# Kernel optimization log

Hardware: AMD Instinct MI355X
Metric: run time of the kernel (lower is better)

The kernel has to match this reference:

```python
import jax, jax.numpy as jnp
import numpy as np

N_NODES = 50000
N_EDGES = 800000
IN_F = 128
HID = 64
HEADS = 4
OUT_F = 16
NEG_SLOPE = 0.2
BN_EPS = 1e-5


def setup_inputs() -> dict:
    key = jax.random.key(0)
    ks = jax.random.split(key, 16)
    g = lambda k, s: (jax.random.normal(k, s, dtype=jnp.float32) * 0.05)
    inp = {
        'x': jax.random.normal(ks[0], (N_NODES, IN_F), dtype=jnp.float32),
        'edge_index': jax.random.randint(ks[1], (2, N_EDGES), 0, N_NODES, dtype=jnp.int64),
        # layer 1: GATConv(128 -> 64, heads=4, concat)
        'W1': g(ks[2], (IN_F, HEADS * HID)),
        'as1': g(ks[3], (HEADS, HID)), 'ad1': g(ks[4], (HEADS, HID)),
        'b1': jnp.zeros((HEADS * HID,), jnp.float32),
        'g1': jnp.ones((HEADS * HID,), jnp.float32), 'be1': jnp.zeros((HEADS * HID,), jnp.float32),
        'm1': jnp.zeros((HEADS * HID,), jnp.float32), 'v1': jnp.ones((HEADS * HID,), jnp.float32),
        # layer 2: GATConv(256 -> 64, heads=4, concat)
        'W2': g(ks[5], (HEADS * HID, HEADS * HID)),
        'as2': g(ks[6], (HEADS, HID)), 'ad2': g(ks[7], (HEADS, HID)),
        'b2': jnp.zeros((HEADS * HID,), jnp.float32),
        'g2': jnp.ones((HEADS * HID,), jnp.float32), 'be2': jnp.zeros((HEADS * HID,), jnp.float32),
        'm2': jnp.zeros((HEADS * HID,), jnp.float32), 'v2': jnp.ones((HEADS * HID,), jnp.float32),
        # layer 3: GATConv(256 -> 16, heads=1, concat=False)
        'W3': g(ks[8], (HEADS * HID, OUT_F)),
        'as3': g(ks[9], (1, OUT_F)), 'ad3': g(ks[10], (1, OUT_F)),
        'b3': jnp.zeros((OUT_F,), jnp.float32),
    }
    return inp


def gat_conv(x, src, dst, W, a_src, a_dst, b, concat):
    n = x.shape[0]
    H, C = a_src.shape
    h = (x @ W).reshape(n, H, C)                       # [N,H,C]
    s_node = jnp.sum(h * a_src[None], axis=-1)         # [N,H]
    d_node = jnp.sum(h * a_dst[None], axis=-1)         # [N,H]
    e = jax.nn.leaky_relu(s_node[src] + d_node[dst], NEG_SLOPE)   # [E,H]
    # segment softmax over incoming edges of each dst node
    e_max = jax.ops.segment_max(e, dst, num_segments=n)
    e_exp = jnp.exp(e - e_max[dst])
    denom = jax.ops.segment_sum(e_exp, dst, num_segments=n)
    alpha = e_exp / denom[dst]                         # [E,H]
    msg = h[src] * alpha[:, :, None]                   # [E,H,C]
    out = jax.ops.segment_sum(msg, dst, num_segments=n)  # [N,H,C]
    out = out.reshape(n, H * C) if concat else out.mean(axis=1)
    return out + b


def batchnorm(x, gamma, beta, mean, var):
    return (x - mean) * jax.lax.rsqrt(var + BN_EPS) * gamma + beta


def reference(x, edge_index, W1, as1, ad1, b1, g1, be1, m1, v1,
              W2, as2, ad2, b2, g2, be2, m2, v2, W3, as3, ad3, b3):
    n = x.shape[0]
    loops = jnp.arange(n, dtype=edge_index.dtype)
    src = jnp.concatenate([edge_index[0], loops])      # PyG add_self_loops
    dst = jnp.concatenate([edge_index[1], loops])
    h = gat_conv(x, src, dst, W1, as1, ad1, b1, concat=True)
    h = jax.nn.relu(batchnorm(h, g1, be1, m1, v1))
    h = gat_conv(h, src, dst, W2, as2, ad2, b2, concat=True)
    h = jax.nn.relu(batchnorm(h, g2, be2, m2, v2))
    out = gat_conv(h, src, dst, W3, as3, ad3, b3, concat=False)
    return out  # out_channels=16 != 1 -> no sigmoid
```

## Files before the change

kernel.cpp:

```cpp
#include <hip/hip_runtime.h>
#include <math.h>

#define NN 50000
#define NE 800000
#define ET (NE + NN)
#define F1 256
#define NEG 0.2f
#define BN_EPS 1e-5f

typedef __attribute__((ext_vector_type(8))) short short8;
typedef __attribute__((ext_vector_type(4))) float float4v;
typedef __attribute__((ext_vector_type(2))) float float2v;
typedef __attribute__((ext_vector_type(4))) unsigned short ushort4v;

__device__ __forceinline__ float bf2f(unsigned short u) {
    unsigned int x = ((unsigned int)u) << 16;
    return __builtin_bit_cast(float, x);
}
__device__ __forceinline__ unsigned short f2bf(float f) {
    unsigned int x = __builtin_bit_cast(unsigned int, f);
    unsigned int lsb = (x >> 16) & 1u;
    x += 0x7fffu + lsb;
    return (unsigned short)(x >> 16);
}
__device__ __forceinline__ unsigned char f2fp8(float f) {
    int p = __builtin_amdgcn_cvt_pk_fp8_f32(f, f, 0, false);
    return (unsigned char)(p & 0xff);
}
__device__ __forceinline__ float lrelu(float x) { return x > 0.f ? x : NEG * x; }

__device__ __forceinline__ void gl_lds16(const unsigned short* g, unsigned short* l) {
    __builtin_amdgcn_global_load_lds((const __attribute__((address_space(1))) void*)g,
                                     (__attribute__((address_space(3))) void*)l, 16, 0, 0);
}

__global__ void prep_all(const float* __restrict__ x, unsigned short* __restrict__ xb,
                         const int* __restrict__ ei, int* __restrict__ counts, int* __restrict__ rank,
                         const float* __restrict__ W1, unsigned short* __restrict__ W1t,
                         const float* __restrict__ W2, unsigned short* __restrict__ W2t,
                         const float* __restrict__ W3, unsigned short* __restrict__ W3h,
                         unsigned short* __restrict__ W3l,
                         const float* __restrict__ b1, const float* __restrict__ g1,
                         const float* __restrict__ be1, const float* __restrict__ m1,
                         const float* __restrict__ v1, float* __restrict__ S1, float* __restrict__ T1,
                         const float* __restrict__ b2, const float* __restrict__ g2,
                         const float* __restrict__ be2, const float* __restrict__ m2,
                         const float* __restrict__ v2, float* __restrict__ S2, float* __restrict__ T2) {
    int blk = blockIdx.x, tid = threadIdx.x;
    if (blk < 6250) {
        int i = blk * 256 + tid;
        float4 v = ((const float4*)x)[i];
        ushort4 o;
        o.x = f2bf(v.x); o.y = f2bf(v.y); o.z = f2bf(v.z); o.w = f2bf(v.w);
        ((ushort4*)xb)[i] = o;
    } else if (blk < 9571) {
        int e = (blk - 6250) * 256 + tid;
        if (e < ET) {
            int dst = (e < NE) ? ei[NE + e] : (e - NE);
            rank[e] = atomicAdd(&counts[dst], 1);
        }
    } else if (blk < 9699) {
        int id = (blk - 9571) * 256 + tid;
        int n = id >> 7, k = id & 127;
        W1t[id] = f2bf(W1[k * 256 + n]);
    } else if (blk < 9955) {
        int id = (blk - 9699) * 256 + tid;
        int n = id >> 8, k = id & 255;
        W2t[id] = f2bf(W2[k * 256 + n]);
    } else if (blk < 9971) {
        int id = (blk - 9955) * 256 + tid;
        int n = id >> 8, k = id & 255;
        float v = W3[k * 16 + n];
        unsigned short hi = f2bf(v);
        W3h[id] = hi;
        W3l[id] = f2bf(v - bf2f(hi));
    } else if (blk == 9971) {
        float s = g1[tid] * rsqrtf(v1[tid] + BN_EPS);
        S1[tid] = s;
        T1[tid] = (b1[tid] - m1[tid]) * s + be1[tid];
    } else {
        float s = g2[tid] * rsqrtf(v2[tid] + BN_EPS);
        S2[tid] = s;
        T2[tid] = (b2[tid] - m2[tid]) * s + be2[tid];
    }
}

__global__ void scan_a(const int* __restrict__ counts, int* __restrict__ rowptr, int* __restrict__ bsum) {
    __shared__ int s[256];
    int t = threadIdx.x, i = blockIdx.x * 256 + t;
    int v = (i < NN) ? counts[i] : 0;
    s[t] = v;
    __syncthreads();
    for (int off = 1; off < 256; off <<= 1) {
        int add = (t >= off) ? s[t - off] : 0;
        __syncthreads();
        s[t] += add;
        __syncthreads();
    }
    if (i < NN) rowptr[i + 1] = s[t];
    if (t == 255) bsum[blockIdx.x] = s[255];
}

__global__ void scan_b(int* __restrict__ bsum, int nb) {
    __shared__ int s[256];
    int t = threadIdx.x;
    int v = (t < nb) ? bsum[t] : 0;
    s[t] = v;
    __syncthreads();
    for (int off = 1; off < 256; off <<= 1) {
        int add = (t >= off) ? s[t - off] : 0;
        __syncthreads();
        s[t] += add;
        __syncthreads();
    }
    if (t < nb) bsum[t] = s[t] - v;
}

__global__ void scan_c(int* __restrict__ rowptr, const int* __restrict__ bsum) {
    int i = blockIdx.x * 256 + threadIdx.x;
    if (i < NN) rowptr[i + 1] += bsum[i >> 8];
    if (i == 0) rowptr[0] = 0;
}

__global__ void edge_place(const int* __restrict__ ei, const int* __restrict__ rowptr,
                           const int* __restrict__ rank, int* __restrict__ csr) {
    int e = blockIdx.x * 256 + threadIdx.x;
    if (e < ET) {
        int src, dst;
        if (e < NE) { src = ei[e]; dst = ei[NE + e]; }
        else        { src = e - NE; dst = src; }
        csr[rowptr[dst] + rank[e]] = src;
    }
}

template<int K, bool F8OUT>
__global__ __launch_bounds__(256, 3) void gemm_lds(const unsigned short* __restrict__ A,
                                                   const unsigned short* __restrict__ Bt,
                                                   void* __restrict__ Cout,
                                                   const float* __restrict__ a_s,
                                                   const float* __restrict__ a_d,
                                                   float* __restrict__ s_arr,
                                                   float* __restrict__ d_arr,
                                                   int M) {
    __shared__ __align__(16) unsigned short As[128 * 64];
    __shared__ __align__(16) unsigned short Bs[128 * 64];
    int tid = threadIdx.x, lane = tid & 63, w = tid >> 6;
    int wr = w >> 1, wc = w & 1;
    int mBase = blockIdx.x * 128, nBase = blockIdx.y * 128;
    int lm = lane & 15, q = lane >> 4;

    float4v acc[4][4];
    for (int i = 0; i < 4; ++i)
        for (int j = 0; j < 4; ++j)
            acc[i][j] = (float4v){0.f, 0.f, 0.f, 0.f};

    const unsigned short* Ap[4];
    const unsigned short* Bp[4];
    for (int p = 0; p < 4; ++p) {
        int slot = p * 256 + tid;
        int row = slot >> 3;
        int csrc = (slot & 7) ^ (row & 7);
        int gm = mBase + row; if (gm >= M) gm = M - 1;
        Ap[p] = A + (size_t)gm * K + csrc * 8;
        Bp[p] = Bt + (size_t)(nBase + row) * K + csrc * 8;
    }

    for (int k0 = 0; k0 < K; k0 += 64) {
        #pragma unroll
        for (int p = 0; p < 4; ++p)
            gl_lds16(Ap[p] + k0, As + ((size_t)p * 256 + w * 64) * 8);
        #pragma unroll
        for (int p = 0; p < 4; ++p)
            gl_lds16(Bp[p] + k0, Bs + ((size_t)p * 256 + w * 64) * 8);
        __syncthreads();
        #pragma unroll
        for (int ks = 0; ks < 64; ks += 32) {
            int cb = ks >> 3;
            short8 af[4], bfr[4];
            #pragma unroll
            for (int i = 0; i < 4; ++i) {
                int row = wr * 64 + i * 16 + lm;
                int ch = (cb + q) ^ (row & 7);
                af[i] = *(const short8*)(As + row * 64 + ch * 8);
            }
            #pragma unroll
            for (int j = 0; j < 4; ++j) {
                int row = wc * 64 + j * 16 + lm;
                int ch = (cb + q) ^ (row & 7);
                bfr[j] = *(const short8*)(Bs + row * 64 + ch * 8);
            }
            #pragma unroll
            for (int i = 0; i < 4; ++i)
                #pragma unroll
                for (int j = 0; j < 4; ++j)
                    acc[i][j] = __builtin_amdgcn_mfma_f32_16x16x32_bf16(af[i], bfr[j], acc[i][j], 0, 0, 0);
        }
        __syncthreads();
    }

    for (int i = 0; i < 4; ++i)
        for (int j = 0; j < 4; ++j) {
            int col = nBase + wc * 64 + j * 16 + lm;
            for (int r = 0; r < 4; ++r) {
                int row = mBase + wr * 64 + i * 16 + q * 4 + r;
                if (row < M) {
                    if constexpr (F8OUT)
                        ((unsigned char*)Cout)[(size_t)row * 256 + col] = f2fp8(acc[i][j][r]);
                    else
                        ((unsigned short*)Cout)[(size_t)row * 256 + col] = f2bf(acc[i][j][r]);
                }
            }
        }
    int head = blockIdx.y * 2 + wc;
    float as_j[4], ad_j[4];
    for (int j = 0; j < 4; ++j) {
        as_j[j] = a_s[head * 64 + j * 16 + lm];
        ad_j[j] = a_d[head * 64 + j * 16 + lm];
    }
    for (int i = 0; i < 4; ++i)
        for (int r = 0; r < 4; ++r) {
            float sp = acc[i][0][r] * as_j[0] + acc[i][1][r] * as_j[1]
                     + acc[i][2][r] * as_j[2] + acc[i][3][r] * as_j[3];
            float dp = acc[i][0][r] * ad_j[0] + acc[i][1][r] * ad_j[1]
                     + acc[i][2][r] * ad_j[2] + acc[i][3][r] * ad_j[3];
            for (int off = 1; off < 16; off <<= 1) {
                sp += __shfl_xor(sp, off);
                dp += __shfl_xor(dp, off);
            }
            int row = mBase + wr * 64 + i * 16 + q * 4 + r;
            if (lm == 0 && row < M) {
                s_arr[row * 4 + head] = sp;
                d_arr[row * 4 + head] = dp;
            }
        }
}

__global__ __launch_bounds__(256) void agg12_f8(const unsigned char* __restrict__ h8,
                                                const float* __restrict__ s_arr, const float* __restrict__ d_arr,
                                                const int* __restrict__ rowptr, const int* __restrict__ csr,
                                                const float* __restrict__ S, const float* __restrict__ T,
                                                unsigned short* __restrict__ out) {
    __shared__ float wls[4][64 * 5];
    int lane = threadIdx.x & 63;
    int wv = threadIdx.x >> 6;
    int node = blockIdx.x * 4 + wv;
    if (node >= NN) return;
    int r0 = rowptr[node], r1 = rowptr[node + 1];
    float4 dv = *(const float4*)(d_arr + node * 4);
    float* wbuf = &wls[wv][0];
    int lp = lane & 31;
    int half = lane >> 5;
    int head8 = lp >> 3;
    const unsigned char* hbase = h8 + lp * 8;

    float2v a01 = {0.f, 0.f}, a23 = {0.f, 0.f}, a45 = {0.f, 0.f}, a67 = {0.f, 0.f};
    float den0 = 0.f, den1 = 0.f, den2 = 0.f, den3 = 0.f;

    for (int base = r0; base < r1; base += 64) {
        int cnt = min(64, r1 - base);
        if (lane < cnt) {
            int src = csr[base + lane];
            float4 sv = *(const float4*)(s_arr + src * 4);
            float w0 = __expf(lrelu(sv.x + dv.x));
            float w1 = __expf(lrelu(sv.y + dv.y));
            float w2 = __expf(lrelu(sv.z + dv.z));
            float w3 = __expf(lrelu(sv.w + dv.w));
            den0 += w0; den1 += w1; den2 += w2; den3 += w3;
            float* wp = wbuf + lane * 5;
            wp[0] = w0; wp[1] = w1; wp[2] = w2; wp[3] = w3;
            wp[4] = __int_as_float(src);
        } else if (lane == cnt) {
            float* wp = wbuf + lane * 5;
            wp[0] = 0.f; wp[1] = 0.f; wp[2] = 0.f; wp[3] = 0.f;
            wp[4] = __int_as_float(node);
        }
        int cpad = (cnt + 1) & ~1;
        for (int k = 0; k < cpad; k += 2) {
            const float* wp = wbuf + (k + half) * 5;
            int src = __float_as_int(wp[4]);
            float wgt = wp[head8];
            uint2 hv = *(const uint2*)(hbase + (size_t)src * 256);
            float2v c0 = __builtin_amdgcn_cvt_pk_f32_fp8((int)hv.x, false);
            float2v c1 = __builtin_amdgcn_cvt_pk_f32_fp8((int)hv.x, true);
            float2v c2 = __builtin_amdgcn_cvt_pk_f32_fp8((int)hv.y, false);
            float2v c3 = __builtin_amdgcn_cvt_pk_f32_fp8((int)hv.y, true);
            float2v w2v = {wgt, wgt};
            a01 += w2v * c0;
            a23 += w2v * c1;
            a45 += w2v * c2;
            a67 += w2v * c3;
        }
    }
    float acc[8] = {a01.x, a01.y, a23.x, a23.y, a45.x, a45.y, a67.x, a67.y};
    for (int u = 0; u < 8; ++u) acc[u] += __shfl_xor(acc[u], 32);
    for (int off = 32; off; off >>= 1) {
        den0 += __shfl_xor(den0, off);
        den1 += __shfl_xor(den1, off);
        den2 += __shfl_xor(den2, off);
        den3 += __shfl_xor(den3, off);
    }
    if (half == 0) {
        float den = (head8 == 0) ? den0 : (head8 == 1) ? den1 : (head8 == 2) ? den2 : den3;
        float inv = 1.f / den;
        int j = lp * 8;
        float4 Sv0 = *(const float4*)(S + j);
        float4 Sv1 = *(const float4*)(S + j + 4);
        float4 Tv0 = *(const float4*)(T + j);
        float4 Tv1 = *(const float4*)(T + j + 4);
        short8 o;
        o[0] = (short)f2bf(fmaxf(acc[0] * inv * Sv0.x + Tv0.x, 0.f));
        o[1] = (short)f2bf(fmaxf(acc[1] * inv * Sv0.y + Tv0.y, 0.f));
        o[2] = (short)f2bf(fmaxf(acc[2] * inv * Sv0.z + Tv0.z, 0.f));
        o[3] = (short)f2bf(fmaxf(acc[3] * inv * Sv0.w + Tv0.w, 0.f));
        o[4] = (short)f2bf(fmaxf(acc[4] * inv * Sv1.x + Tv1.x, 0.f));
        o[5] = (short)f2bf(fmaxf(acc[5] * inv * Sv1.y + Tv1.y, 0.f));
        o[6] = (short)f2bf(fmaxf(acc[6] * inv * Sv1.z + Tv1.z, 0.f));
        o[7] = (short)f2bf(fmaxf(acc[7] * inv * Sv1.w + Tv1.w, 0.f));
        *(short8*)(out + (size_t)node * F1 + j) = o;
    }
}

__global__ __launch_bounds__(256) void agg12(const unsigned short* __restrict__ h,
                                             const float* __restrict__ s_arr, const float* __restrict__ d_arr,
                                             const int* __restrict__ rowptr, const int* __restrict__ csr,
                                             const float* __restrict__ S, const float* __restrict__ T,
                                             unsigned short* __restrict__ out) {
    __shared__ float wls[4][64 * 5];
    int lane = threadIdx.x & 63;
    int wv = threadIdx.x >> 6;
    int node = blockIdx.x * 4 + wv;
    if (node >= NN) return;
    int r0 = rowptr[node], r1 = rowptr[node + 1];
    float4 dv = *(const float4*)(d_arr + node * 4);
    float* wbuf = &wls[wv][0];
    int lp = lane & 31;
    int half = lane >> 5;
    int head8 = lp >> 3;
    const unsigned short* hbase = h + lp * 8;

    float acc[8] = {0.f, 0.f, 0.f, 0.f, 0.f, 0.f, 0.f, 0.f};
    float den0 = 0.f, den1 = 0.f, den2 = 0.f, den3 = 0.f;

    for (int base = r0; base < r1; base += 64) {
        int cnt = min(64, r1 - base);
        if (lane < cnt) {
            int src = csr[base + lane];
            float4 sv = *(const float4*)(s_arr + src * 4);
            float w0 = __expf(lrelu(sv.x + dv.x));
            float w1 = __expf(lrelu(sv.y + dv.y));
            float w2 = __expf(lrelu(sv.z + dv.z));
            float w3 = __expf(lrelu(sv.w + dv.w));
            den0 += w0; den1 += w1; den2 += w2; den3 += w3;
            float* wp = wbuf + lane * 5;
            wp[0] = w0; wp[1] = w1; wp[2] = w2; wp[3] = w3;
            wp[4] = __int_as_float(src);
        } else if (lane == cnt) {
            float* wp = wbuf + lane * 5;
            wp[0] = 0.f; wp[1] = 0.f; wp[2] = 0.f; wp[3] = 0.f;
            wp[4] = __int_as_float(node);
        }
        int cpad = (cnt + 1) & ~1;
        for (int k = 0; k < cpad; k += 2) {
            const float* wp = wbuf + (k + half) * 5;
            int src = __float_as_int(wp[4]);
            float wgt = wp[head8];
            short8 hv = *(const short8*)(hbase + (size_t)src * F1);
            acc[0] += wgt * bf2f((unsigned short)hv[0]);
            acc[1] += wgt * bf2f((unsigned short)hv[1]);
            acc[2] += wgt * bf2f((unsigned short)hv[2]);
            acc[3] += wgt * bf2f((unsigned short)hv[3]);
            acc[4] += wgt * bf2f((unsigned short)hv[4]);
            acc[5] += wgt * bf2f((unsigned short)hv[5]);
            acc[6] += wgt * bf2f((unsigned short)hv[6]);
            acc[7] += wgt * bf2f((unsigned short)hv[7]);
        }
    }
    for (int u = 0; u < 8; ++u) acc[u] += __shfl_xor(acc[u], 32);
    for (int off = 32; off; off >>= 1) {
        den0 += __shfl_xor(den0, off);
        den1 += __shfl_xor(den1, off);
        den2 += __shfl_xor(den2, off);
        den3 += __shfl_xor(den3, off);
    }
    if (half == 0) {
        float den = (head8 == 0) ? den0 : (head8 == 1) ? den1 : (head8 == 2) ? den2 : den3;
        float inv = 1.f / den;
        int j = lp * 8;
        float4 Sv0 = *(const float4*)(S + j);
        float4 Sv1 = *(const float4*)(S + j + 4);
        float4 Tv0 = *(const float4*)(T + j);
        float4 Tv1 = *(const float4*)(T + j + 4);
        short8 o;
        o[0] = (short)f2bf(fmaxf(acc[0] * inv * Sv0.x + Tv0.x, 0.f));
        o[1] = (short)f2bf(fmaxf(acc[1] * inv * Sv0.y + Tv0.y, 0.f));
        o[2] = (short)f2bf(fmaxf(acc[2] * inv * Sv0.z + Tv0.z, 0.f));
        o[3] = (short)f2bf(fmaxf(acc[3] * inv * Sv0.w + Tv0.w, 0.f));
        o[4] = (short)f2bf(fmaxf(acc[4] * inv * Sv1.x + Tv1.x, 0.f));
        o[5] = (short)f2bf(fmaxf(acc[5] * inv * Sv1.y + Tv1.y, 0.f));
        o[6] = (short)f2bf(fmaxf(acc[6] * inv * Sv1.z + Tv1.z, 0.f));
        o[7] = (short)f2bf(fmaxf(acc[7] * inv * Sv1.w + Tv1.w, 0.f));
        *(short8*)(out + (size_t)node * F1 + j) = o;
    }
}

__global__ __launch_bounds__(256) void gemm3_mfma(const unsigned short* __restrict__ A,
                                                  const unsigned short* __restrict__ W3h,
                                                  const unsigned short* __restrict__ W3l,
                                                  const float* __restrict__ as3, const float* __restrict__ ad3,
                                                  float* __restrict__ h3, float* __restrict__ s3,
                                                  float* __restrict__ d3, int M) {
    int tid = threadIdx.x, lane = tid & 63, w = tid >> 6;
    int mBase = blockIdx.x * 64 + w * 16;
    int lm = lane & 15, q = lane >> 4;
    int row = mBase + lm;
    int rc = (row < M) ? row : (M - 1);
    const unsigned short* pA = A + (size_t)rc * 256 + q * 8;
    const unsigned short* pH = W3h + lm * 256 + q * 8;
    const unsigned short* pL = W3l + lm * 256 + q * 8;
    float4v acc = (float4v){0.f, 0.f, 0.f, 0.f};
    #pragma unroll
    for (int s = 0; s < 8; ++s) {
        short8 a  = *(const short8*)(pA + s * 32);
        short8 bh = *(const short8*)(pH + s * 32);
        short8 bl = *(const short8*)(pL + s * 32);
        acc = __builtin_amdgcn_mfma_f32_16x16x32_bf16(a, bh, acc, 0, 0, 0);
        acc = __builtin_amdgcn_mfma_f32_16x16x32_bf16(a, bl, acc, 0, 0, 0);
    }
    float a_s = as3[lm], a_d = ad3[lm];
    for (int r = 0; r < 4; ++r) {
        int rw = mBase + q * 4 + r;
        if (rw < M) h3[(size_t)rw * 16 + lm] = acc[r];
        float sp = acc[r] * a_s, dp = acc[r] * a_d;
        for (int off = 1; off < 16; off <<= 1) {
            sp += __shfl_xor(sp, off);
            dp += __shfl_xor(dp, off);
        }
        if (lm == 0 && rw < M) { s3[rw] = sp; d3[rw] = dp; }
    }
}

__global__ __launch_bounds__(256) void agg3(const float* __restrict__ h3, const float* __restrict__ s3,
                                            const float* __restrict__ d3, const int* __restrict__ rowptr,
                                            const int* __restrict__ csr, const float* __restrict__ b3,
                                            float* __restrict__ out) {
    int lane = threadIdx.x & 63;
    int node = blockIdx.x * 4 + (threadIdx.x >> 6);
    if (node >= NN) return;
    int r0 = rowptr[node], r1 = rowptr[node + 1];
    float dv = d3[node];
    int c = lane & 15, g = lane >> 4;
    float acc = 0.f, den = 0.f;
    for (int e = r0 + g; e < r1; e += 4) {
        int src = csr[e];
        float w = __expf(lrelu(s3[src] + dv));
        den += w;
        acc += w * h3[(size_t)src * 16 + c];
    }
    acc += __shfl_xor(acc, 16); acc += __shfl_xor(acc, 32);
    den += __shfl_xor(den, 16); den += __shfl_xor(den, 32);
    if (lane < 16) out[(size_t)node * 16 + lane] = acc / den + b3[lane];
}

extern "C" void kernel_launch(void* const* d_in, const int* in_sizes, int n_in,
                              void* d_out, int out_size, void* d_ws, size_t ws_size,
                              hipStream_t stream) {
    const float* x   = (const float*)d_in[0];
    const int*   ei  = (const int*)d_in[1];
    const float* W1  = (const float*)d_in[2];
    const float* as1 = (const float*)d_in[3];
    const float* ad1 = (const float*)d_in[4];
    const float* b1  = (const float*)d_in[5];
    const float* g1  = (const float*)d_in[6];
    const float* be1 = (const float*)d_in[7];
    const float* m1  = (const float*)d_in[8];
    const float* v1  = (const float*)d_in[9];
    const float* W2  = (const float*)d_in[10];
    const float* as2 = (const float*)d_in[11];
    const float* ad2 = (const float*)d_in[12];
    const float* b2  = (const float*)d_in[13];
    const float* g2  = (const float*)d_in[14];
    const float* be2 = (const float*)d_in[15];
    const float* m2  = (const float*)d_in[16];
    const float* v2  = (const float*)d_in[17];
    const float* W3  = (const float*)d_in[18];
    const float* as3 = (const float*)d_in[19];
    const float* ad3 = (const float*)d_in[20];
    const float* b3  = (const float*)d_in[21];

    char* w = (char*)d_ws;
    size_t off = 0;
    auto alloc = [&](size_t bytes) -> void* {
        off = (off + 255) & ~(size_t)255;
        void* p = w + off;
        off += bytes;
        return p;
    };
    unsigned short* xb    = (unsigned short*)alloc((size_t)NN * 128 * 2);
    unsigned short* W1t   = (unsigned short*)alloc(256 * 128 * 2);
    unsigned short* W2t   = (unsigned short*)alloc(256 * 256 * 2);
    unsigned short* W3h   = (unsigned short*)alloc(16 * 256 * 2);
    unsigned short* W3l   = (unsigned short*)alloc(16 * 256 * 2);
    unsigned char*  Abuf8 = (unsigned char*)alloc((size_t)NN * F1);
    unsigned short* Abuf  = (unsigned short*)alloc((size_t)NN * F1 * 2);
    unsigned short* Bbuf  = (unsigned short*)alloc((size_t)NN * F1 * 2);
    float* h3    = (float*)alloc((size_t)NN * 16 * 4);
    float* s_arr = (float*)alloc((size_t)NN * 4 * 4);
    float* d_arr = (float*)alloc((size_t)NN * 4 * 4);
    float* s3    = (float*)alloc((size_t)NN * 4);
    float* d3    = (float*)alloc((size_t)NN * 4);
    int* counts  = (int*)alloc((size_t)NN * 4);
    int* rowptr  = (int*)alloc((size_t)(NN + 1) * 4);
    int* rank    = (int*)alloc((size_t)ET * 4);
    int* csr     = (int*)alloc((size_t)ET * 4);
    int* bsum    = (int*)alloc(256 * 4);
    float* S1 = (float*)alloc(F1 * 4);
    float* T1 = (float*)alloc(F1 * 4);
    float* S2 = (float*)alloc(F1 * 4);
    float* T2 = (float*)alloc(F1 * 4);
    float* outp = (float*)d_out;

    int nb_scan = (NN + 255) / 256;
    int nb_edge = (ET + 255) / 256;

    hipMemsetAsync(counts, 0, (size_t)NN * 4, stream);
    prep_all<<<9973, 256, 0, stream>>>(x, xb, ei, counts, rank,
                                       W1, W1t, W2, W2t, W3, W3h, W3l,
                                       b1, g1, be1, m1, v1, S1, T1,
                                       b2, g2, be2, m2, v2, S2, T2);
    scan_a<<<nb_scan, 256, 0, stream>>>(counts, rowptr, bsum);
    scan_b<<<1, 256, 0, stream>>>(bsum, nb_scan);
    scan_c<<<nb_scan, 256, 0, stream>>>(rowptr, bsum);
    edge_place<<<nb_edge, 256, 0, stream>>>(ei, rowptr, rank, csr);

    dim3 ggrid((NN + 127) / 128, 2);
    int agrid = (NN + 3) / 4;

    gemm_lds<128, true><<<ggrid, 256, 0, stream>>>(xb, W1t, Abuf8, as1, ad1, s_arr, d_arr, NN);
    agg12_f8<<<agrid, 256, 0, stream>>>(Abuf8, s_arr, d_arr, rowptr, csr, S1, T1, Bbuf);

    gemm_lds<256, false><<<ggrid, 256, 0, stream>>>(Bbuf, W2t, Abuf, as2, ad2, s_arr, d_arr, NN);
    agg12<<<agrid, 256, 0, stream>>>(Abuf, s_arr, d_arr, rowptr, csr, S2, T2, Bbuf);

    gemm3_mfma<<<(NN + 63) / 64, 256, 0, stream>>>(Bbuf, W3h, W3l, as3, ad3, h3, s3, d3, NN);
    agg3<<<agrid, 256, 0, stream>>>(h3, s3, d3, rowptr, csr, b3, outp);
}
```

Before: 356.0 us.

## Unroll edge gathers two-deep in aggregation kernels, stage agg3 weights, merge scans

The aggregation loops in agg12_f8 and agg12 now process two edge pairs per iteration, issuing two independent feature gathers before accumulating. The goal is more memory-level parallelism on the latency-bound random reads. agg3 is restructured so each wave computes the edge weights once per lane into LDS and then gathers h3 rows two at a time, instead of recomputing the exp per feature lane. The scan_b and scan_c launches are merged into one kernel that reduces the preceding block sums itself, removing one launch. Padding rises to multiples of 4 or 8, which adds some wasted gathers of the node's own row.

Result: faster. 345.2 us, median of 2 (-3.0%).

```diff
diff --git a/kernel.cpp b/kernel.cpp
--- a/kernel.cpp
+++ b/kernel.cpp
@@ -101,24 +101,18 @@
     if (t == 255) bsum[blockIdx.x] = s[255];
 }
 
-__global__ void scan_b(int* __restrict__ bsum, int nb) {
+__global__ void scan_bc(int* __restrict__ rowptr, const int* __restrict__ bsum, int nb) {
     __shared__ int s[256];
-    int t = threadIdx.x;
-    int v = (t < nb) ? bsum[t] : 0;
-    s[t] = v;
+    int t = threadIdx.x, bid = blockIdx.x;
+    s[t] = (t < bid && t < nb) ? bsum[t] : 0;
     __syncthreads();
-    for (int off = 1; off < 256; off <<= 1) {
-        int add = (t >= off) ? s[t - off] : 0;
+    for (int off = 128; off; off >>= 1) {
+        if (t < off) s[t] += s[t + off];
         __syncthreads();
-        s[t] += add;
-        __syncthreads();
-    }
-    if (t < nb) bsum[t] = s[t] - v;
-}
-
-__global__ void scan_c(int* __restrict__ rowptr, const int* __restrict__ bsum) {
-    int i = blockIdx.x * 256 + threadIdx.x;
-    if (i < NN) rowptr[i + 1] += bsum[i >> 8];
+    }
+    int add = s[0];
+    int i = bid * 256 + t;
+    if (i < NN) rowptr[i + 1] += add;
     if (i == 0) rowptr[0] = 0;
 }
 
@@ -258,6 +252,7 @@
 
     for (int base = r0; base < r1; base += 64) {
         int cnt = min(64, r1 - base);
+        int cpad = (cnt + 3) & ~3;
         if (lane < cnt) {
             int src = csr[base + lane];
             float4 sv = *(const float4*)(s_arr + src * 4);
@@ -269,26 +264,29 @@
             float* wp = wbuf + lane * 5;
             wp[0] = w0; wp[1] = w1; wp[2] = w2; wp[3] = w3;
             wp[4] = __int_as_float(src);
-        } else if (lane == cnt) {
+        } else if (lane < cpad) {
             float* wp = wbuf + lane * 5;
             wp[0] = 0.f; wp[1] = 0.f; wp[2] = 0.f; wp[3] = 0.f;
             wp[4] = __int_as_float(node);
         }
-        int cpad = (cnt + 1) & ~1;
-        for (int k = 0; k < cpad; k += 2) {
-            const float* wp = wbuf + (k + half) * 5;
-            int src = __float_as_int(wp[4]);
-            float wgt = wp[head8];
-            uint2 hv = *(const uint2*)(hbase + (size_t)src * 256);
-            float2v c0 = __builtin_amdgcn_cvt_pk_f32_fp8((int)hv.x, false);
-            float2v c1 = __builtin_amdgcn_cvt_pk_f32_fp8((int)hv.x, true);
-            float2v c2 = __builtin_amdgcn_cvt_pk_f32_fp8((int)hv.y, false);
-            float2v c3 = __builtin_amdgcn_cvt_pk_f32_fp8((int)hv.y, true);
-            float2v w2v = {wgt, wgt};
-            a01 += w2v * c0;
-            a23 += w2v * c1;
-            a45 += w2v * c2;
-            a67 += w2v * c3;
+        for (int k = 0; k < cpad; k += 4) {
+            const float* wpA = wbuf + (k + half) * 5;
+            const float* wpB = wpA + 10;
+            int srcA = __float_as_int(wpA[4]);
+            int srcB = __float_as_int(wpB[4]);
+            float wgtA = wpA[head8];
+            float wgtB = wpB[head8];
+            uint2 hvA = *(const uint2*)(hbase + (size_t)srcA * 256);
+            uint2 hvB = *(const uint2*)(hbase + (size_t)srcB * 256);
+            float2v wA = {wgtA, wgtA}, wB = {wgtB, wgtB};
+            a01 += wA * __builtin_amdgcn_cvt_pk_f32_fp8((int)hvA.x, false);
+            a23 += wA * __builtin_amdgcn_cvt_pk_f32_fp8((int)hvA.x, true);
+            a45 += wA * __builtin_amdgcn_cvt_pk_f32_fp8((int)hvA.y, false);
+            a67 += wA * __builtin_amdgcn_cvt_pk_f32_fp8((int)hvA.y, true);
+            a01 += wB * __builtin_amdgcn_cvt_pk_f32_fp8((int)hvB.x, false);
+            a23 += wB * __builtin_amdgcn_cvt_pk_f32_fp8((int)hvB.x, true);
+            a45 += wB * __builtin_amdgcn_cvt_pk_f32_fp8((int)hvB.y, false);
+            a67 += wB * __builtin_amdgcn_cvt_pk_f32_fp8((int)hvB.y, true);
         }
     }
     float acc[8] = {a01.x, a01.y, a23.x, a23.y, a45.x, a45.y, a67.x, a67.y};
@@ -343,6 +341,7 @@
 
     for (int base = r0; base < r1; base += 64) {
         int cnt = min(64, r1 - base);
+        int cpad = (cnt + 3) & ~3;
         if (lane < cnt) {
             int src = csr[base + lane];
             float4 sv = *(const float4*)(s_arr + src * 4);
@@ -354,25 +353,36 @@
             float* wp = wbuf + lane * 5;
             wp[0] = w0; wp[1] = w1; wp[2] = w2; wp[3] = w3;
             wp[4] = __int_as_float(src);
-        } else if (lane == cnt) {
+        } else if (lane < cpad) {
             float* wp = wbuf + lane * 5;
             wp[0] = 0.f; wp[1] = 0.f; wp[2] = 0.f; wp[3] = 0.f;
             wp[4] = __int_as_float(node);
         }
-        int cpad = (cnt + 1) & ~1;
-        for (int k = 0; k < cpad; k += 2) {
-            const float* wp = wbuf + (k + half) * 5;
-            int src = __float_as_int(wp[4]);
-            float wgt = wp[head8];
-            short8 hv = *(const short8*)(hbase + (size_t)src * F1);
-            acc[0] += wgt * bf2f((unsigned short)hv[0]);
-            acc[1] += wgt * bf2f((unsigned short)hv[1]);
-            acc[2] += wgt * bf2f((unsigned short)hv[2]);
-            acc[3] += wgt * bf2f((unsigned short)hv[3]);
-            acc[4] += wgt * bf2f((unsigned short)hv[4]);
-            acc[5] += wgt * bf2f((unsigned short)hv[5]);
-            acc[6] += wgt * bf2f((unsigned short)hv[6]);
-            acc[7] += wgt * bf2f((unsigned short)hv[7]);
+        for (int k = 0; k < cpad; k += 4) {
+            const float* wpA = wbuf + (k + half) * 5;
+            const float* wpB = wpA + 10;
+            int srcA = __float_as_int(wpA[4]);
+            int srcB = __float_as_int(wpB[4]);
+            float wgtA = wpA[head8];
+            float wgtB = wpB[head8];
+            short8 hvA = *(const short8*)(hbase + (size_t)srcA * F1);
+            short8 hvB = *(const short8*)(hbase + (size_t)srcB * F1);
+            acc[0] += wgtA * bf2f((unsigned short)hvA[0]);
+            acc[1] += wgtA * bf2f((unsigned short)hvA[1]);
+            acc[2] += wgtA * bf2f((unsigned short)hvA[2]);
+            acc[3] += wgtA * bf2f((unsigned short)hvA[3]);
+            acc[4] += wgtA * bf2f((unsigned short)hvA[4]);
+            acc[5] += wgtA * bf2f((unsigned short)hvA[5]);
+            acc[6] += wgtA * bf2f((unsigned short)hvA[6]);
+            acc[7] += wgtA * bf2f((unsigned short)hvA[7]);
+            acc[0] += wgtB * bf2f((unsigned short)hvB[0]);
+            acc[1] += wgtB * bf2f((unsigned short)hvB[1]);
+            acc[2] += wgtB * bf2f((unsigned short)hvB[2]);
+            acc[3] += wgtB * bf2f((unsigned short)hvB[3]);
+            acc[4] += wgtB * bf2f((unsigned short)hvB[4]);
+            acc[5] += wgtB * bf2f((unsigned short)hvB[5]);
+            acc[6] += wgtB * bf2f((unsigned short)hvB[6]);
+            acc[7] += wgtB * bf2f((unsigned short)hvB[7]);
         }
     }
     for (int u = 0; u < 8; ++u) acc[u] += __shfl_xor(acc[u], 32);
@@ -443,21 +453,42 @@
                                             const float* __restrict__ d3, const int* __restrict__ rowptr,
                                             const int* __restrict__ csr, const float* __restrict__ b3,
                                             float* __restrict__ out) {
+    __shared__ float wls[4][64 * 2];
     int lane = threadIdx.x & 63;
-    int node = blockIdx.x * 4 + (threadIdx.x >> 6);
+    int wv = threadIdx.x >> 6;
+    int node = blockIdx.x * 4 + wv;
     if (node >= NN) return;
     int r0 = rowptr[node], r1 = rowptr[node + 1];
     float dv = d3[node];
+    float* wbuf = &wls[wv][0];
     int c = lane & 15, g = lane >> 4;
     float acc = 0.f, den = 0.f;
-    for (int e = r0 + g; e < r1; e += 4) {
-        int src = csr[e];
-        float w = __expf(lrelu(s3[src] + dv));
-        den += w;
-        acc += w * h3[(size_t)src * 16 + c];
+    for (int base = r0; base < r1; base += 64) {
+        int cnt = min(64, r1 - base);
+        int cpad = (cnt + 7) & ~7;
+        if (lane < cnt) {
+            int src = csr[base + lane];
+            float w = __expf(lrelu(s3[src] + dv));
+            den += w;
+            wbuf[lane * 2] = w;
+            wbuf[lane * 2 + 1] = __int_as_float(src);
+        } else if (lane < cpad) {
+            wbuf[lane * 2] = 0.f;
+            wbuf[lane * 2 + 1] = __int_as_float(node);
+        }
+        for (int k = 0; k < cpad; k += 8) {
+            const float* wpA = wbuf + (k + g) * 2;
+            const float* wpB = wpA + 8;
+            float wA = wpA[0]; int sA = __float_as_int(wpA[1]);
+            float wB = wpB[0]; int sB = __float_as_int(wpB[1]);
+            float hA = h3[(size_t)sA * 16 + c];
+            float hB = h3[(size_t)sB * 16 + c];
+            acc += wA * hA;
+            acc += wB * hB;
+        }
     }
     acc += __shfl_xor(acc, 16); acc += __shfl_xor(acc, 32);
-    den += __shfl_xor(den, 16); den += __shfl_xor(den, 32);
+    for (int off = 32; off; off >>= 1) den += __shfl_xor(den, off);
     if (lane < 16) out[(size_t)node * 16 + lane] = acc / den + b3[lane];
 }
 
@@ -528,8 +559,7 @@
                                        b1, g1, be1, m1, v1, S1, T1,
                                        b2, g2, be2, m2, v2, S2, T2);
     scan_a<<<nb_scan, 256, 0, stream>>>(counts, rowptr, bsum);
-    scan_b<<<1, 256, 0, stream>>>(bsum, nb_scan);
-    scan_c<<<nb_scan, 256, 0, stream>>>(rowptr, bsum);
+    scan_bc<<<nb_scan, 256, 0, stream>>>(rowptr, bsum, nb_scan);
     edge_place<<<nb_edge, 256, 0, stream>>>(ei, rowptr, rank, csr);
 
     dim3 ggrid((NN + 127) / 128, 2);
```
